# Optimization experiments

Measured on AMD Instinct MI355X. Metric: run time of the kernel, lower is better.

The kernel has to match this reference:

```python
import jax, jax.numpy as jnp
import numpy as np

B, T, D, H = 2, 2048, 1024, 16
HD = D // H  # 64


def setup_inputs() -> dict:
    key = jax.random.key(0)
    ks = jax.random.split(key, 4)
    x = jax.random.normal(ks[0], (B, T, D), dtype=jnp.float32)
    mask = jnp.ones((1, 1, T, T), dtype=jnp.int32)
    w_qkv = jax.random.normal(ks[1], (3 * D, D), dtype=jnp.float32) * (1.0 / np.sqrt(D))
    b_qkv = jnp.zeros((3 * D,), dtype=jnp.float32)
    w_out = jax.random.normal(ks[2], (D, D), dtype=jnp.float32) * (1.0 / np.sqrt(D))
    b_out = jnp.zeros((D,), dtype=jnp.float32)
    return {"x": x, "mask": mask, "w_qkv": w_qkv, "b_qkv": b_qkv,
            "w_out": w_out, "b_out": b_out}


def reference(x, mask, w_qkv, b_qkv, w_out, b_out):
    b, t, d = x.shape
    # qkv projection (torch Linear: x @ W.T + b) -> [b, t, 3, H, HD]
    qkv = (x @ w_qkv.T + b_qkv).reshape(b, t, 3, H, HD)
    q, k, v = qkv[:, :, 0], qkv[:, :, 1], qkv[:, :, 2]  # each [b, t, H, HD]
    scale = 1.0 / np.sqrt(HD).astype(np.float32)
    # scores: [b, H, t, t]
    scores = jnp.einsum('bqhd,bkhd->bhqk', q, k) * scale
    scores = jnp.where(mask == 0, -jnp.inf, scores)
    attn = jax.nn.softmax(scores, axis=-1)
    y = jnp.einsum('bhqk,bkhd->bqhd', attn, v).reshape(b, t, d)
    return y @ w_out.T + b_out
```

## Files before the change

kernel.cpp:

```cpp
#include <hip/hip_runtime.h>
#include <stdint.h>

typedef unsigned short u16;
typedef __attribute__((ext_vector_type(8))) short bf16x8;
typedef bf16x8 __attribute__((may_alias)) bf16x8_a;
typedef __attribute__((ext_vector_type(4))) float f32x4;
typedef f32x4 __attribute__((may_alias)) f32x4_a;

#define GLOBAL_AS __attribute__((address_space(1)))
#define LDS_AS    __attribute__((address_space(3)))

#define NB 2
#define NT 2048
#define ND 1024
#define NH 16
#define NHD 64
#define SCALE_LOG2E 0.1803368801111f

static __device__ __forceinline__ u16 f2b(float f) {
  uint32_t x = __builtin_bit_cast(uint32_t, f);
  x += 0x7fffu + ((x >> 16) & 1u);
  return (u16)(x >> 16);
}

static __device__ __forceinline__ void async16(const u16* g, u16* l) {
  __builtin_amdgcn_global_load_lds((const GLOBAL_AS uint32_t*)g, (LDS_AS uint32_t*)l, 16, 0, 0);
}

__global__ __launch_bounds__(256)
void cvt_bf16(const float* __restrict__ src, u16* __restrict__ dst, int n8) {
  const int i = blockIdx.x * blockDim.x + threadIdx.x;
  if (i < n8) {
    const f32x4 a = ((const f32x4_a*)src)[2 * i];
    const f32x4 b = ((const f32x4_a*)src)[2 * i + 1];
    bf16x8 o;
#pragma unroll
    for (int e = 0; e < 4; ++e) {
      ((short*)&o)[e]     = (short)f2b(a[e]);
      ((short*)&o)[e + 4] = (short)f2b(b[e]);
    }
    ((bf16x8_a*)dst)[i] = o;
  }
}

template <int MODE>
__global__ __launch_bounds__(256, 2)
void gemm128(const u16* __restrict__ A, const u16* __restrict__ W,
             const float* __restrict__ bias, void* __restrict__ Cv) {
  constexpr int K = 1024;
  __shared__ alignas(16) u16 As[128 * 64];
  __shared__ alignas(16) u16 Bs[128 * 64];

  const int tid  = threadIdx.x;
  const int lane = tid & 63;
  const int wave = tid >> 6;
  const int l16  = lane & 15;
  const int quad = lane >> 4;
  const int row0 = blockIdx.x * 128;
  const int col0 = blockIdx.y * 128;
  const int wm   = (wave >> 1) * 64;
  const int wn   = (wave & 1) * 64;

  const f32x4 z4 = {0.f, 0.f, 0.f, 0.f};
  f32x4 acc[4][4];
#pragma unroll
  for (int i = 0; i < 4; ++i)
#pragma unroll
    for (int j = 0; j < 4; ++j) acc[i][j] = z4;

  for (int k0 = 0; k0 < K; k0 += 64) {
    __syncthreads();
#pragma unroll
    for (int t = 0; t < 4; ++t) {
      const int cbase = wave * 64 + t * 256;
      const int L   = cbase + lane;
      const int row = L >> 3;
      const int h8  = (L - row) & 7;
      async16(A + (size_t)(row0 + row) * K + k0 + h8 * 8, As + cbase * 8);
      async16(W + (size_t)(col0 + row) * K + k0 + h8 * 8, Bs + cbase * 8);
    }
    __syncthreads();

#pragma unroll
    for (int ks = 0; ks < 2; ++ks) {
      const int c = ks * 4 + quad;
      bf16x8 af[4], bfr[4];
#pragma unroll
      for (int i = 0; i < 4; ++i) {
        const int m = wm + i * 16 + l16;
        af[i] = *(const bf16x8_a*)(As + m * 64 + ((c + m) & 7) * 8);
      }
#pragma unroll
      for (int j = 0; j < 4; ++j) {
        const int n = wn + j * 16 + l16;
        bfr[j] = *(const bf16x8_a*)(Bs + n * 64 + ((c + n) & 7) * 8);
      }
#pragma unroll
      for (int i = 0; i < 4; ++i)
#pragma unroll
        for (int j = 0; j < 4; ++j)
          acc[i][j] = __builtin_amdgcn_mfma_f32_16x16x32_bf16(af[i], bfr[j], acc[i][j], 0, 0, 0);
    }
  }

#pragma unroll
  for (int j = 0; j < 4; ++j) {
    const int n = col0 + wn + j * 16 + l16;
    const float bn = bias[n];
    if (MODE == 0) {
      u16* C = (u16*)Cv;
      const int s  = n >> 10;
      const int h  = (n >> 6) & (NH - 1);
      const int hd = n & (NHD - 1);
      u16* dst = C + (size_t)s * (NB * NH * NT * NHD);
#pragma unroll
      for (int i = 0; i < 4; ++i)
#pragma unroll
        for (int r = 0; r < 4; ++r) {
          const int m = row0 + wm + i * 16 + quad * 4 + r;
          const int b = m >> 11, t = m & (NT - 1);
          const size_t idx = (s == 2)
              ? (((size_t)(b * NH + h) * NHD + hd) * NT + t)
              : ((((size_t)b * NH + h) * NT + t) * NHD + hd);
          dst[idx] = f2b(acc[i][j][r] + bn);
        }
    } else {
      float* C = (float*)Cv;
#pragma unroll
      for (int i = 0; i < 4; ++i)
#pragma unroll
        for (int r = 0; r < 4; ++r) {
          const int m = row0 + wm + i * 16 + quad * 4 + r;
          C[(size_t)m * ND + n] = acc[i][j][r] + bn;
        }
    }
  }
}

__global__ __launch_bounds__(256, 2)
void attn(const u16* __restrict__ Qb, const u16* __restrict__ Kb,
          const u16* __restrict__ Vb, u16* __restrict__ Yb) {
  __shared__ alignas(16) u16 Ks[2][64 * 64];
  __shared__ alignas(16) u16 Vt[2][64 * 64];
  __shared__ alignas(16) u16 Ps[4][32 * 72];

  const int tid  = threadIdx.x;
  const int lane = tid & 63;
  const int wave = tid >> 6;
  const int l16  = lane & 15;
  const int quad = lane >> 4;

  const int bh = blockIdx.x;
  const int q0 = blockIdx.y * 128;
  const u16* Q  = Qb + (size_t)bh * NT * NHD;
  const u16* Kg = Kb + (size_t)bh * NT * NHD;
  const u16* Vg = Vb + (size_t)bh * NHD * NT;
  const int b = bh >> 4, h = bh & (NH - 1);
  u16* Y = Yb + (size_t)b * NT * ND + h * NHD;

  const int qw = q0 + wave * 32;

  bf16x8 qf[2][2];
#pragma unroll
  for (int i = 0; i < 2; ++i)
#pragma unroll
    for (int ks = 0; ks < 2; ++ks)
      qf[i][ks] = *(const bf16x8_a*)(Q + (size_t)(qw + i * 16 + l16) * NHD + ks * 32 + quad * 8);

  const f32x4 z4 = {0.f, 0.f, 0.f, 0.f};
  f32x4 o[2][4];
  float lacc[2][4];
#pragma unroll
  for (int i = 0; i < 2; ++i) {
#pragma unroll
    for (int n = 0; n < 4; ++n) o[i][n] = z4;
#pragma unroll
    for (int r = 0; r < 4; ++r) lacc[i][r] = 0.f;
  }
  u16* Pw = &Ps[wave][0];

  auto stage = [&](int key0, int buf) {
#pragma unroll
    for (int cc = 0; cc < 2; ++cc) {
      const int cbase = wave * 64 + cc * 256;
      const int L   = cbase + lane;
      const int row = L >> 3;
      const int h8  = (L - row) & 7;
      async16(Kg + (size_t)(key0 + row) * NHD + h8 * 8, &Ks[buf][0] + cbase * 8);
      async16(Vg + (size_t)row * NT + key0 + h8 * 8, &Vt[buf][0] + cbase * 8);
    }
  };

  stage(0, 0);
  __syncthreads();

  for (int kb = 0; kb < NT / 64; ++kb) {
    const int buf = kb & 1;
    if (kb + 1 < NT / 64) stage((kb + 1) * 64, buf ^ 1);

    f32x4 s[2][4];
#pragma unroll
    for (int i = 0; i < 2; ++i)
#pragma unroll
      for (int n = 0; n < 4; ++n) s[i][n] = z4;
#pragma unroll
    for (int ks = 0; ks < 2; ++ks) {
      const int c = ks * 4 + quad;
      bf16x8 kf[4];
#pragma unroll
      for (int n = 0; n < 4; ++n) {
        const int key = n * 16 + l16;
        kf[n] = *(const bf16x8_a*)(&Ks[buf][0] + key * 64 + ((c + key) & 7) * 8);
      }
#pragma unroll
      for (int i = 0; i < 2; ++i)
#pragma unroll
        for (int n = 0; n < 4; ++n)
          s[i][n] = __builtin_amdgcn_mfma_f32_16x16x32_bf16(qf[i][ks], kf[n], s[i][n], 0, 0, 0);
    }

#pragma unroll
    for (int i = 0; i < 2; ++i)
#pragma unroll
      for (int r = 0; r < 4; ++r) {
        float rs = 0.f;
#pragma unroll
        for (int n = 0; n < 4; ++n) {
          const float p = __builtin_amdgcn_exp2f(s[i][n][r] * SCALE_LOG2E);
          s[i][n][r] = p;
          rs += p;
        }
        lacc[i][r] += rs;
      }

#pragma unroll
    for (int i = 0; i < 2; ++i)
#pragma unroll
      for (int n = 0; n < 4; ++n)
#pragma unroll
        for (int r = 0; r < 4; ++r)
          Pw[(i * 16 + quad * 4 + r) * 72 + n * 16 + l16] = f2b(s[i][n][r]);

#pragma unroll
    for (int ks = 0; ks < 2; ++ks) {
      const int c = ks * 4 + quad;
      bf16x8 pf[2], vf[4];
#pragma unroll
      for (int i = 0; i < 2; ++i)
        pf[i] = *(const bf16x8_a*)(Pw + (i * 16 + l16) * 72 + ks * 32 + quad * 8);
#pragma unroll
      for (int n = 0; n < 4; ++n) {
        const int hd = n * 16 + l16;
        vf[n] = *(const bf16x8_a*)(&Vt[buf][0] + hd * 64 + ((c + hd) & 7) * 8);
      }
#pragma unroll
      for (int i = 0; i < 2; ++i)
#pragma unroll
        for (int n = 0; n < 4; ++n)
          o[i][n] = __builtin_amdgcn_mfma_f32_16x16x32_bf16(pf[i], vf[n], o[i][n], 0, 0, 0);
    }

    __syncthreads();
  }

#pragma unroll
  for (int i = 0; i < 2; ++i)
#pragma unroll
    for (int r = 0; r < 4; ++r) {
      float l = lacc[i][r];
      l += __shfl_xor(l, 1);
      l += __shfl_xor(l, 2);
      l += __shfl_xor(l, 4);
      l += __shfl_xor(l, 8);
      const float inv = 1.0f / l;
      const int t = qw + i * 16 + quad * 4 + r;
#pragma unroll
      for (int n = 0; n < 4; ++n)
        Y[(size_t)t * ND + n * 16 + l16] = f2b(o[i][n][r] * inv);
    }
}

extern "C" void kernel_launch(void* const* d_in, const int* in_sizes, int n_in,
                              void* d_out, int out_size, void* d_ws, size_t ws_size,
                              hipStream_t stream) {
  const float* x     = (const float*)d_in[0];
  const float* w_qkv = (const float*)d_in[2];
  const float* b_qkv = (const float*)d_in[3];
  const float* w_out = (const float*)d_in[4];
  const float* b_out = (const float*)d_in[5];

  u16* ws = (u16*)d_ws;
  const size_t perbuf = (size_t)NB * NH * NT * NHD;
  u16* qkv   = ws;
  u16* xb    = ws + 3 * perbuf;
  u16* y     = xb;
  u16* wqkvb = ws + 4 * perbuf;
  u16* woutb = wqkvb + (size_t)3 * ND * ND;

  dim3 blk(256);
  cvt_bf16<<<dim3(2048), blk, 0, stream>>>(x, xb, 524288);
  cvt_bf16<<<dim3(1536), blk, 0, stream>>>(w_qkv, wqkvb, 393216);
  cvt_bf16<<<dim3(512),  blk, 0, stream>>>(w_out, woutb, 131072);

  gemm128<0><<<dim3(32, 24), blk, 0, stream>>>(xb, wqkvb, b_qkv, qkv);
  attn<<<dim3(32, 16), blk, 0, stream>>>(qkv, qkv + perbuf, qkv + 2 * perbuf, y);
  gemm128<1><<<dim3(32, 8), blk, 0, stream>>>(y, woutb, b_out, d_out);
}
```

Before: 216.8 us.

## Halve attention query tile, swizzle P buffer, and fuse bf16 conversion launches

The attention kernel now gives each block 64 queries (16 per wave) instead of 128, which doubles the grid to 1024 blocks and raises the occupancy hint to 4 blocks per CU. The per-wave P scratch buffer moves from a padded layout to an XOR-style swizzled 16x64 layout to avoid LDS bank conflicts. The three fp32-to-bf16 conversion launches are merged into one kernel to cut launch overhead. The trade-off is that every block still streams all K/V tiles, so K/V LDS traffic per query doubles and each wave issues fewer MFMAs per K/V fragment load.

```diff
diff --git a/kernel.cpp b/kernel.cpp
--- a/kernel.cpp
+++ b/kernel.cpp
@@ -27,20 +27,28 @@
   __builtin_amdgcn_global_load_lds((const GLOBAL_AS uint32_t*)g, (LDS_AS uint32_t*)l, 16, 0, 0);
 }
 
+#define XN8   524288
+#define WQN8  393216
+#define WON8  131072
 __global__ __launch_bounds__(256)
-void cvt_bf16(const float* __restrict__ src, u16* __restrict__ dst, int n8) {
-  const int i = blockIdx.x * blockDim.x + threadIdx.x;
-  if (i < n8) {
-    const f32x4 a = ((const f32x4_a*)src)[2 * i];
-    const f32x4 b = ((const f32x4_a*)src)[2 * i + 1];
-    bf16x8 o;
-#pragma unroll
-    for (int e = 0; e < 4; ++e) {
-      ((short*)&o)[e]     = (short)f2b(a[e]);
-      ((short*)&o)[e + 4] = (short)f2b(b[e]);
-    }
-    ((bf16x8_a*)dst)[i] = o;
-  }
+void cvt_all(const float* __restrict__ x, const float* __restrict__ wq,
+             const float* __restrict__ wo, u16* __restrict__ xb,
+             u16* __restrict__ wqb, u16* __restrict__ wob) {
+  int i = blockIdx.x * blockDim.x + threadIdx.x;
+  const float* src;
+  u16* dst;
+  if (i < XN8)              { src = x;  dst = xb; }
+  else if (i < XN8 + WQN8)  { src = wq; dst = wqb; i -= XN8; }
+  else                      { src = wo; dst = wob; i -= XN8 + WQN8; }
+  const f32x4 a = ((const f32x4_a*)src)[2 * i];
+  const f32x4 b = ((const f32x4_a*)src)[2 * i + 1];
+  bf16x8 o;
+#pragma unroll
+  for (int e = 0; e < 4; ++e) {
+    ((short*)&o)[e]     = (short)f2b(a[e]);
+    ((short*)&o)[e + 4] = (short)f2b(b[e]);
+  }
+  ((bf16x8_a*)dst)[i] = o;
 }
 
 template <int MODE>
@@ -137,12 +145,12 @@
   }
 }
 
-__global__ __launch_bounds__(256, 2)
+__global__ __launch_bounds__(256, 4)
 void attn(const u16* __restrict__ Qb, const u16* __restrict__ Kb,
           const u16* __restrict__ Vb, u16* __restrict__ Yb) {
   __shared__ alignas(16) u16 Ks[2][64 * 64];
   __shared__ alignas(16) u16 Vt[2][64 * 64];
-  __shared__ alignas(16) u16 Ps[4][32 * 72];
+  __shared__ alignas(16) u16 Ps[4][16 * 64];
 
   const int tid  = threadIdx.x;
   const int lane = tid & 63;
@@ -151,32 +159,27 @@
   const int quad = lane >> 4;
 
   const int bh = blockIdx.x;
-  const int q0 = blockIdx.y * 128;
+  const int q0 = blockIdx.y * 64;
   const u16* Q  = Qb + (size_t)bh * NT * NHD;
   const u16* Kg = Kb + (size_t)bh * NT * NHD;
   const u16* Vg = Vb + (size_t)bh * NHD * NT;
   const int b = bh >> 4, h = bh & (NH - 1);
   u16* Y = Yb + (size_t)b * NT * ND + h * NHD;
 
-  const int qw = q0 + wave * 32;
-
-  bf16x8 qf[2][2];
-#pragma unroll
-  for (int i = 0; i < 2; ++i)
-#pragma unroll
-    for (int ks = 0; ks < 2; ++ks)
-      qf[i][ks] = *(const bf16x8_a*)(Q + (size_t)(qw + i * 16 + l16) * NHD + ks * 32 + quad * 8);
+  const int qw = q0 + wave * 16;
+
+  bf16x8 qf[2];
+#pragma unroll
+  for (int ks = 0; ks < 2; ++ks)
+    qf[ks] = *(const bf16x8_a*)(Q + (size_t)(qw + l16) * NHD + ks * 32 + quad * 8);
 
   const f32x4 z4 = {0.f, 0.f, 0.f, 0.f};
-  f32x4 o[2][4];
-  float lacc[2][4];
-#pragma unroll
-  for (int i = 0; i < 2; ++i) {
-#pragma unroll
-    for (int n = 0; n < 4; ++n) o[i][n] = z4;
-#pragma unroll
-    for (int r = 0; r < 4; ++r) lacc[i][r] = 0.f;
-  }
+  f32x4 o[4];
+  float lacc[4];
+#pragma unroll
+  for (int n = 0; n < 4; ++n) o[n] = z4;
+#pragma unroll
+  for (int r = 0; r < 4; ++r) lacc[r] = 0.f;
   u16* Pw = &Ps[wave][0];
 
   auto stage = [&](int key0, int buf) {
@@ -198,11 +201,9 @@
     const int buf = kb & 1;
     if (kb + 1 < NT / 64) stage((kb + 1) * 64, buf ^ 1);
 
-    f32x4 s[2][4];
-#pragma unroll
-    for (int i = 0; i < 2; ++i)
-#pragma unroll
-      for (int n = 0; n < 4; ++n) s[i][n] = z4;
+    f32x4 s[4];
+#pragma unroll
+    for (int n = 0; n < 4; ++n) s[n] = z4;
 #pragma unroll
     for (int ks = 0; ks < 2; ++ks) {
       const int c = ks * 4 + quad;
@@ -213,71 +214,63 @@
         kf[n] = *(const bf16x8_a*)(&Ks[buf][0] + key * 64 + ((c + key) & 7) * 8);
       }
 #pragma unroll
-      for (int i = 0; i < 2; ++i)
-#pragma unroll
-        for (int n = 0; n < 4; ++n)
-          s[i][n] = __builtin_amdgcn_mfma_f32_16x16x32_bf16(qf[i][ks], kf[n], s[i][n], 0, 0, 0);
-    }
-
-#pragma unroll
-    for (int i = 0; i < 2; ++i)
+      for (int n = 0; n < 4; ++n)
+        s[n] = __builtin_amdgcn_mfma_f32_16x16x32_bf16(qf[ks], kf[n], s[n], 0, 0, 0);
+    }
+
+#pragma unroll
+    for (int r = 0; r < 4; ++r) {
+      float rs = 0.f;
+#pragma unroll
+      for (int n = 0; n < 4; ++n) {
+        const float p = __builtin_amdgcn_exp2f(s[n][r] * SCALE_LOG2E);
+        s[n][r] = p;
+        rs += p;
+      }
+      lacc[r] += rs;
+    }
+
+#pragma unroll
+    for (int n = 0; n < 4; ++n) {
+      const int chunk = n * 2 + (l16 >> 3);
 #pragma unroll
       for (int r = 0; r < 4; ++r) {
-        float rs = 0.f;
-#pragma unroll
-        for (int n = 0; n < 4; ++n) {
-          const float p = __builtin_amdgcn_exp2f(s[i][n][r] * SCALE_LOG2E);
-          s[i][n][r] = p;
-          rs += p;
-        }
-        lacc[i][r] += rs;
-      }
-
-#pragma unroll
-    for (int i = 0; i < 2; ++i)
-#pragma unroll
-      for (int n = 0; n < 4; ++n)
-#pragma unroll
-        for (int r = 0; r < 4; ++r)
-          Pw[(i * 16 + quad * 4 + r) * 72 + n * 16 + l16] = f2b(s[i][n][r]);
+        const int row = quad * 4 + r;
+        Pw[row * 64 + ((chunk + row) & 7) * 8 + (l16 & 7)] = f2b(s[n][r]);
+      }
+    }
 
 #pragma unroll
     for (int ks = 0; ks < 2; ++ks) {
       const int c = ks * 4 + quad;
-      bf16x8 pf[2], vf[4];
-#pragma unroll
-      for (int i = 0; i < 2; ++i)
-        pf[i] = *(const bf16x8_a*)(Pw + (i * 16 + l16) * 72 + ks * 32 + quad * 8);
+      bf16x8 pf, vf[4];
+      pf = *(const bf16x8_a*)(Pw + l16 * 64 + ((c + l16) & 7) * 8);
 #pragma unroll
       for (int n = 0; n < 4; ++n) {
         const int hd = n * 16 + l16;
         vf[n] = *(const bf16x8_a*)(&Vt[buf][0] + hd * 64 + ((c + hd) & 7) * 8);
       }
 #pragma unroll
-      for (int i = 0; i < 2; ++i)
-#pragma unroll
-        for (int n = 0; n < 4; ++n)
-          o[i][n] = __builtin_amdgcn_mfma_f32_16x16x32_bf16(pf[i], vf[n], o[i][n], 0, 0, 0);
+      for (int n = 0; n < 4; ++n)
+        o[n] = __builtin_amdgcn_mfma_f32_16x16x32_bf16(pf, vf[n], o[n], 0, 0, 0);
     }
 
     __syncthreads();
   }
 
 #pragma unroll
-  for (int i = 0; i < 2; ++i)
-#pragma unroll
-    for (int r = 0; r < 4; ++r) {
-      float l = lacc[i][r];
-      l += __shfl_xor(l, 1);
-      l += __shfl_xor(l, 2);
-      l += __shfl_xor(l, 4);
-      l += __shfl_xor(l, 8);
-      const float inv = 1.0f / l;
-      const int t = qw + i * 16 + quad * 4 + r;
-#pragma unroll
-      for (int n = 0; n < 4; ++n)
-        Y[(size_t)t * ND + n * 16 + l16] = f2b(o[i][n][r] * inv);
-    }
+  for (int r = 0; r < 4; ++r) {
+    float l = lacc[r];
+    l += __shfl_xor(l, 1);
+    l += __shfl_xor(l, 2);
+    l += __shfl_xor(l, 4);
+    l += __shfl_xor(l, 8);
+    const float inv = 1.0f / l;
+    const int t = qw + quad * 4 + r;
+#pragma unroll
+    for (int n = 0; n < 4; ++n)
+      Y[(size_t)t * ND + n * 16 + l16] = f2b(o[n][r] * inv);
+  }
 }
 
 extern "C" void kernel_launch(void* const* d_in, const int* in_sizes, int n_in,
@@ -298,11 +291,8 @@
   u16* woutb = wqkvb + (size_t)3 * ND * ND;
 
   dim3 blk(256);
-  cvt_bf16<<<dim3(2048), blk, 0, stream>>>(x, xb, 524288);
-  cvt_bf16<<<dim3(1536), blk, 0, stream>>>(w_qkv, wqkvb, 393216);
-  cvt_bf16<<<dim3(512),  blk, 0, stream>>>(w_out, woutb, 131072);
-
+  cvt_all<<<dim3(4096), blk, 0, stream>>>(x, w_qkv, w_out, xb, wqkvb, woutb);
   gemm128<0><<<dim3(32, 24), blk, 0, stream>>>(xb, wqkvb, b_qkv, qkv);
-  attn<<<dim3(32, 16), blk, 0, stream>>>(qkv, qkv + perbuf, qkv + 2 * perbuf, y);
+  attn<<<dim3(32, 32), blk, 0, stream>>>(qkv, qkv + perbuf, qkv + 2 * perbuf, y);
   gemm128<1><<<dim3(32, 8), blk, 0, stream>>>(y, woutb, b_out, d_out);
 }
```

After: 213.5 us. About the same (-1.6%).
